# Optimization experiments

Hardware: AMD Instinct MI355X
Metric: run time of the kernel (lower is better)

The kernel has to match this reference:

```python
import jax, jax.numpy as jnp
import numpy as np

NUM_HEADS = 16

def setup_inputs() -> dict:
    key = jax.random.key(0)
    ks = jax.random.split(key, 5)
    b, n, d = 2, 2048, 1024
    s = 0.02
    return {
        "x": jax.random.normal(ks[0], (b, n, d), jnp.float32),
        "wq": jax.random.normal(ks[1], (d, d), jnp.float32) * s,
        "wk": jax.random.normal(ks[2], (d, d), jnp.float32) * s,
        "wv": jax.random.normal(ks[3], (d, d), jnp.float32) * s,
        "wo": jax.random.normal(ks[4], (d, d), jnp.float32) * s,
        "bo": jnp.zeros((d,), jnp.float32),
    }

def reference(x, wq, wk, wv, wo, bo):
    b, n, c = x.shape
    h = NUM_HEADS
    hd = c // h
    scale = hd ** -0.5
    # qkv projections (qkv_bias=False); torch Linear computes x @ W.T
    def split_heads(t):
        return t.reshape(b, n, h, hd).transpose(0, 2, 1, 3)  # b h n d
    q = split_heads(x @ wq.T)
    k = split_heads(x @ wk.T)
    v = split_heads(x @ wv.T)
    dots = jnp.einsum('bhid,bhjd->bhij', q, k) * scale
    attn = jax.nn.softmax(dots, axis=-1)  # attn_drop=0 -> identity
    out = jnp.einsum('bhij,bhjd->bhid', attn, v)
    out = out.transpose(0, 2, 1, 3).reshape(b, n, c)
    out = out @ wo.T + bo  # proj_drop=0 -> identity
    return out
```

## Files before the change

### kernel.cpp

```cpp
#include <hip/hip_runtime.h>
#include <hip/hip_bf16.h>

typedef float f32x4 __attribute__((ext_vector_type(4)));
typedef short short8 __attribute__((ext_vector_type(8)));
typedef short short4v __attribute__((ext_vector_type(4)));

#define MFMA(a, b, c) __builtin_amdgcn_mfma_f32_16x16x32_bf16((a), (b), (c), 0, 0, 0)

#if __has_builtin(__builtin_amdgcn_exp2f)
#define EXP2(x) __builtin_amdgcn_exp2f(x)
#else
#define EXP2(x) exp2f(x)
#endif

#define B_  2
#define N_  2048
#define C_  1024
#define H_  16
#define HD_ 64
#define M_  (B_ * N_)

#define QSCALE 0.18033688011112042f

typedef const __attribute__((address_space(1))) void* gp_t;
typedef __attribute__((address_space(3))) void* sp_t;
#define GLL16(g, s) __builtin_amdgcn_global_load_lds((gp_t)(const void*)(g), (sp_t)(void*)(s), 16, 0, 0)

__device__ __forceinline__ short f2bf(float f) {
    union { float fv; unsigned u; } v; v.fv = f;
    unsigned r = v.u + 0x7fffu + ((v.u >> 16) & 1u);
    return (short)(r >> 16);
}
__device__ __forceinline__ unsigned pack_rne(float a, float b) {
    return (unsigned)(unsigned short)f2bf(a) | ((unsigned)(unsigned short)f2bf(b) << 16);
}

__global__ __launch_bounds__(256) void convert_kernel(
    const float* __restrict__ x,  const float* __restrict__ wq,
    const float* __restrict__ wk, const float* __restrict__ wv,
    const float* __restrict__ wo, short* __restrict__ dst)
{
    size_t e = ((size_t)blockIdx.x * 256 + threadIdx.x) * 8;
    const float* src; size_t off;
    if (e < 4194304)      { src = x;  off = e; }
    else if (e < 5242880) { src = wq; off = e - 4194304; }
    else if (e < 6291456) { src = wk; off = e - 5242880; }
    else if (e < 7340032) { src = wv; off = e - 6291456; }
    else                  { src = wo; off = e - 7340032; }
    float4 a = *(const float4*)(src + off);
    float4 b = *(const float4*)(src + off + 4);
    short8 s;
    s[0] = f2bf(a.x); s[1] = f2bf(a.y); s[2] = f2bf(a.z); s[3] = f2bf(a.w);
    s[4] = f2bf(b.x); s[5] = f2bf(b.y); s[6] = f2bf(b.z); s[7] = f2bf(b.w);
    *(short8*)(dst + e) = s;
}

__global__ __launch_bounds__(256) void qkv_gemm(
    const short* __restrict__ xb, const short* __restrict__ Wb,
    short* __restrict__ Qb, short* __restrict__ Kb, short* __restrict__ Vt)
{
    const int m0 = blockIdx.x * 128;
    const int n0 = blockIdx.y * 128;
    __shared__ short As[128 * 32];
    __shared__ short Bs[128 * 32];
    const int tid  = threadIdx.x;
    const int wave = tid >> 6, lane = tid & 63;
    const int quad = lane >> 4, l16 = lane & 15;
    const int wr = (wave >> 1) * 64, wc = (wave & 1) * 64;

    f32x4 acc[4][4] = {};

    for (int kk = 0; kk < C_; kk += 32) {
        __syncthreads();
        #pragma unroll
        for (int it = 0; it < 2; ++it) {
            int f = (it * 256 + tid) * 8;
            int row = f >> 5, col = f & 31;
            GLL16(xb + (size_t)(m0 + row) * C_ + kk + col, &As[f]);
            GLL16(Wb + (size_t)(n0 + row) * C_ + kk + col, &Bs[f]);
        }
        __syncthreads();
        short8 af[4], bf[4];
        #pragma unroll
        for (int mi = 0; mi < 4; ++mi) af[mi] = *(const short8*)&As[(wr + mi * 16 + l16) * 32 + quad * 8];
        #pragma unroll
        for (int ni = 0; ni < 4; ++ni) bf[ni] = *(const short8*)&Bs[(wc + ni * 16 + l16) * 32 + quad * 8];
        #pragma unroll
        for (int mi = 0; mi < 4; ++mi)
        #pragma unroll
        for (int ni = 0; ni < 4; ++ni)
            acc[mi][ni] = MFMA(af[mi], bf[ni], acc[mi][ni]);
    }

    const int which = n0 >> 10;
    const int nb = n0 & 1023;
    #pragma unroll
    for (int mi = 0; mi < 4; ++mi)
    #pragma unroll
    for (int ni = 0; ni < 4; ++ni)
    #pragma unroll
    for (int r = 0; r < 4; ++r) {
        int m  = m0 + wr + mi * 16 + quad * 4 + r;
        int cc = nb + wc + ni * 16 + l16;
        float av = acc[mi][ni][r];
        if (which == 0) av *= QSCALE;
        short bv = f2bf(av);
        int bb = m >> 11, ns = m & (N_ - 1);
        int h = cc >> 6, d = cc & 63;
        size_t bh = (size_t)(bb * H_ + h);
        if (which == 0)      Qb[(bh * N_ + ns) * HD_ + d] = bv;
        else if (which == 1) Kb[(bh * N_ + ns) * HD_ + d] = bv;
        else                 Vt[(bh * HD_ + d) * N_ + ns] = bv;
    }
}

__global__ __launch_bounds__(256, 2) void attn_kernel(
    const short* __restrict__ Qb, const short* __restrict__ Kb,
    const short* __restrict__ Vt, short* __restrict__ Ob)
{
    const int bh = blockIdx.y;
    const int b = bh >> 4, h = bh & (H_ - 1);
    const int i0 = blockIdx.x * 128;
    __shared__ short Qs[128 * 64];
    __shared__ short Ks[2][64 * 64];
    __shared__ short Vs[2][64 * 64];
    const int tid  = threadIdx.x;
    const int wave = tid >> 6, lane = tid & 63;
    const int quad = lane >> 4, l16 = lane & 15;
    const int sw = l16 & 7;

    const short* Qg = Qb + ((size_t)bh * N_ + i0) * HD_;
    const short* Kg = Kb + (size_t)bh * N_ * HD_;
    const short* Vg = Vt + (size_t)bh * HD_ * N_;

    const int row0 = tid >> 3,  c0 = (tid & 7) ^ (row0 & 7);
    const int row1 = row0 + 32, c1 = (tid & 7) ^ (row1 & 7);
    const short* KgA0 = Kg + row0 * HD_ + c0 * 8;
    const short* KgA1 = Kg + row1 * HD_ + c1 * 8;
    const short* VgA0 = Vg + (size_t)row0 * N_ + c0 * 8;
    const short* VgA1 = Vg + (size_t)row1 * N_ + c1 * 8;

    #pragma unroll
    for (int it = 0; it < 4; ++it) {
        int s = it * 256 + tid;
        int row = s >> 3, c = (s & 7) ^ (row & 7);
        GLL16(Qg + row * HD_ + c * 8, &Qs[s * 8]);
    }
    GLL16(KgA0, &Ks[0][tid * 8]);
    GLL16(KgA1, &Ks[0][(tid + 256) * 8]);
    GLL16(VgA0, &Vs[0][tid * 8]);
    GLL16(VgA1, &Vs[0][(tid + 256) * 8]);
    __syncthreads();

    short8 qf[2][2];
    #pragma unroll
    for (int s = 0; s < 2; ++s) {
        int row = (wave * 32 + s * 16 + l16) * 64;
        qf[s][0] = *(const short8*)&Qs[row + ((quad ^ sw) * 8)];
        qf[s][1] = *(const short8*)&Qs[row + (((quad + 4) ^ sw) * 8)];
    }

    f32x4 o[2][4] = {};
    float lrow[2] = {0.f, 0.f};

    for (int jt = 0; jt < N_ / 64; ++jt) {
        const int cur = jt & 1;
        if (jt + 1 < N_ / 64) {
            int j1 = (jt + 1) * 64;
            GLL16(KgA0 + (size_t)j1 * HD_, &Ks[cur ^ 1][tid * 8]);
            GLL16(KgA1 + (size_t)j1 * HD_, &Ks[cur ^ 1][(tid + 256) * 8]);
            GLL16(VgA0 + j1, &Vs[cur ^ 1][tid * 8]);
            GLL16(VgA1 + j1, &Vs[cur ^ 1][(tid + 256) * 8]);
        }
        const short* Kc = Ks[cur];
        const short* Vc = Vs[cur];

        #pragma unroll
        for (int half = 0; half < 2; ++half) {
            unsigned pq[2][4];
            #pragma unroll
            for (int nio = 0; nio < 2; ++nio) {
                int ni = half * 2 + nio;
                int krow = (ni * 16 + l16) * 64;
                short8 kf0 = *(const short8*)&Kc[krow + ((quad ^ sw) * 8)];
                short8 kf1 = *(const short8*)&Kc[krow + (((quad + 4) ^ sw) * 8)];
                #pragma unroll
                for (int s = 0; s < 2; ++s) {
                    f32x4 st = {0.f, 0.f, 0.f, 0.f};
                    st = MFMA(kf0, qf[s][0], st);
                    st = MFMA(kf1, qf[s][1], st);
                    union { float f; unsigned u; } e0, e1, e2, e3;
                    e0.f = EXP2(st[0]); e1.f = EXP2(st[1]);
                    e2.f = EXP2(st[2]); e3.f = EXP2(st[3]);
                    lrow[s] += (e0.f + e1.f) + (e2.f + e3.f);
                    pq[s][nio * 2]     = (e0.u >> 16) | (e1.u & 0xffff0000u);
                    pq[s][nio * 2 + 1] = (e2.u >> 16) | (e3.u & 0xffff0000u);
                }
            }
            #pragma unroll
            for (int di = 0; di < 4; ++di) {
                int vrow = (di * 16 + l16) * 64;
                int ch1 = (half * 4 +     (quad >> 1)) ^ sw;
                int ch2 = (half * 4 + 2 + (quad >> 1)) ^ sw;
                union { struct { short4v lo, hi; } p; short8 v; } va;
                va.p.lo = *(const short4v*)&Vc[vrow + ch1 * 8 + (quad & 1) * 4];
                va.p.hi = *(const short4v*)&Vc[vrow + ch2 * 8 + (quad & 1) * 4];
                #pragma unroll
                for (int s = 0; s < 2; ++s) {
                    union { unsigned u[4]; short8 v; } pb;
                    pb.u[0] = pq[s][0]; pb.u[1] = pq[s][1];
                    pb.u[2] = pq[s][2]; pb.u[3] = pq[s][3];
                    o[s][di] = MFMA(va.v, pb.v, o[s][di]);
                }
            }
        }
        __syncthreads();
    }

    #pragma unroll
    for (int s = 0; s < 2; ++s) {
        float l = lrow[s];
        l += __shfl_xor(l, 16, 64);
        l += __shfl_xor(l, 32, 64);
        float inv = 1.f / l;
        int ig = i0 + wave * 32 + s * 16 + l16;
        size_t base = ((size_t)(b * N_ + ig)) * C_ + h * HD_;
        #pragma unroll
        for (int di = 0; di < 4; ++di) {
            unsigned p01 = pack_rne(o[s][di][0] * inv, o[s][di][1] * inv);
            unsigned p23 = pack_rne(o[s][di][2] * inv, o[s][di][3] * inv);
            *(unsigned*)&Ob[base + di * 16 + quad * 4]     = p01;
            *(unsigned*)&Ob[base + di * 16 + quad * 4 + 2] = p23;
        }
    }
}

__global__ __launch_bounds__(256) void proj_gemm(
    const short* __restrict__ Ob, const short* __restrict__ wob,
    const float* __restrict__ bo, float* __restrict__ out)
{
    const int m0 = blockIdx.x * 64;
    const int n0 = blockIdx.y * 128;
    __shared__ short As[64 * 32];
    __shared__ short Bs[128 * 32];
    const int tid  = threadIdx.x;
    const int wave = tid >> 6, lane = tid & 63;
    const int quad = lane >> 4, l16 = lane & 15;
    const int wr = (wave >> 1) * 32, wc = (wave & 1) * 64;

    f32x4 acc[2][4] = {};

    for (int kk = 0; kk < C_; kk += 32) {
        __syncthreads();
        {
            int f = tid * 8;
            int row = f >> 5, col = f & 31;
            GLL16(Ob + (size_t)(m0 + row) * C_ + kk + col, &As[f]);
        }
        #pragma unroll
        for (int it = 0; it < 2; ++it) {
            int f = (it * 256 + tid) * 8;
            int row = f >> 5, col = f & 31;
            GLL16(wob + (size_t)(n0 + row) * C_ + kk + col, &Bs[f]);
        }
        __syncthreads();
        short8 af[2], bf[4];
        #pragma unroll
        for (int mi = 0; mi < 2; ++mi) af[mi] = *(const short8*)&As[(wr + mi * 16 + l16) * 32 + quad * 8];
        #pragma unroll
        for (int ni = 0; ni < 4; ++ni) bf[ni] = *(const short8*)&Bs[(wc + ni * 16 + l16) * 32 + quad * 8];
        #pragma unroll
        for (int mi = 0; mi < 2; ++mi)
        #pragma unroll
        for (int ni = 0; ni < 4; ++ni)
            acc[mi][ni] = MFMA(af[mi], bf[ni], acc[mi][ni]);
    }

    #pragma unroll
    for (int mi = 0; mi < 2; ++mi)
    #pragma unroll
    for (int ni = 0; ni < 4; ++ni)
    #pragma unroll
    for (int r = 0; r < 4; ++r) {
        int m = m0 + wr + mi * 16 + quad * 4 + r;
        int c = n0 + wc + ni * 16 + l16;
        out[(size_t)m * C_ + c] = acc[mi][ni][r] + bo[c];
    }
}

extern "C" void kernel_launch(void* const* d_in, const int* in_sizes, int n_in,
                              void* d_out, int out_size, void* d_ws, size_t ws_size,
                              hipStream_t stream) {
    const float* x  = (const float*)d_in[0];
    const float* wq = (const float*)d_in[1];
    const float* wk = (const float*)d_in[2];
    const float* wv = (const float*)d_in[3];
    const float* wo = (const float*)d_in[4];
    const float* bo = (const float*)d_in[5];
    float* out = (float*)d_out;

    short* xb  = (short*)d_ws;
    short* Wb  = xb  + 4194304;
    short* wob = Wb  + 3145728;
    short* Qb  = wob + 1048576;
    short* Kb  = Qb  + 4194304;
    short* Vt  = Kb  + 4194304;
    short* Obuf= Vt  + 4194304;

    dim3 blk(256);
    convert_kernel<<<4096, blk, 0, stream>>>(x, wq, wk, wv, wo, xb);
    qkv_gemm<<<dim3(M_ / 128, 3072 / 128), blk, 0, stream>>>(xb, Wb, Qb, Kb, Vt);
    attn_kernel<<<dim3(N_ / 128, B_ * H_), blk, 0, stream>>>(Qb, Kb, Vt, Obuf);
    proj_gemm<<<dim3(M_ / 64, C_ / 128), blk, 0, stream>>>(Obuf, wob, bo, out);
}
```

Measured before the change: 190.9 us.

## Split attention over key halves and split-K the output projection

```diff
diff --git a/kernel.cpp b/kernel.cpp
--- a/kernel.cpp
+++ b/kernel.cpp
@@ -114,16 +114,19 @@
     }
 }
 
-__global__ __launch_bounds__(256, 2) void attn_kernel(
+__global__ __launch_bounds__(256, 4) void attn_kernel(
     const short* __restrict__ Qb, const short* __restrict__ Kb,
-    const short* __restrict__ Vt, short* __restrict__ Ob)
+    const short* __restrict__ Vt, short* __restrict__ op0,
+    short* __restrict__ op1, float* __restrict__ lb)
 {
     const int bh = blockIdx.y;
     const int b = bh >> 4, h = bh & (H_ - 1);
     const int i0 = blockIdx.x * 128;
-    __shared__ short Qs[128 * 64];
+    const int half = blockIdx.z;
+    const int jzb = half * (N_ / 2);
     __shared__ short Ks[2][64 * 64];
     __shared__ short Vs[2][64 * 64];
+    short* const Qs = &Ks[0][0];
     const int tid  = threadIdx.x;
     const int wave = tid >> 6, lane = tid & 63;
     const int quad = lane >> 4, l16 = lane & 15;
@@ -135,10 +138,10 @@
 
     const int row0 = tid >> 3,  c0 = (tid & 7) ^ (row0 & 7);
     const int row1 = row0 + 32, c1 = (tid & 7) ^ (row1 & 7);
-    const short* KgA0 = Kg + row0 * HD_ + c0 * 8;
-    const short* KgA1 = Kg + row1 * HD_ + c1 * 8;
-    const short* VgA0 = Vg + (size_t)row0 * N_ + c0 * 8;
-    const short* VgA1 = Vg + (size_t)row1 * N_ + c1 * 8;
+    const short* KgA0 = Kg + (size_t)(jzb + row0) * HD_ + c0 * 8;
+    const short* KgA1 = Kg + (size_t)(jzb + row1) * HD_ + c1 * 8;
+    const short* VgA0 = Vg + (size_t)row0 * N_ + jzb + c0 * 8;
+    const short* VgA1 = Vg + (size_t)row1 * N_ + jzb + c1 * 8;
 
     #pragma unroll
     for (int it = 0; it < 4; ++it) {
@@ -146,26 +149,29 @@
         int row = s >> 3, c = (s & 7) ^ (row & 7);
         GLL16(Qg + row * HD_ + c * 8, &Qs[s * 8]);
     }
+    __syncthreads();
+    short8 qf[2][2];
+    #pragma unroll
+    for (int s = 0; s < 2; ++s) {
+        int row = (wave * 32 + s * 16 + l16) * 64;
+        qf[s][0] = *(const short8*)&Qs[row + ((quad ^ sw) * 8)];
+        qf[s][1] = *(const short8*)&Qs[row + (((quad + 4) ^ sw) * 8)];
+    }
+    __syncthreads();
+
     GLL16(KgA0, &Ks[0][tid * 8]);
     GLL16(KgA1, &Ks[0][(tid + 256) * 8]);
     GLL16(VgA0, &Vs[0][tid * 8]);
     GLL16(VgA1, &Vs[0][(tid + 256) * 8]);
     __syncthreads();
 
-    short8 qf[2][2];
-    #pragma unroll
-    for (int s = 0; s < 2; ++s) {
-        int row = (wave * 32 + s * 16 + l16) * 64;
-        qf[s][0] = *(const short8*)&Qs[row + ((quad ^ sw) * 8)];
-        qf[s][1] = *(const short8*)&Qs[row + (((quad + 4) ^ sw) * 8)];
-    }
-
     f32x4 o[2][4] = {};
     float lrow[2] = {0.f, 0.f};
-
-    for (int jt = 0; jt < N_ / 64; ++jt) {
+    const int NT = (N_ / 2) / 64;
+
+    for (int jt = 0; jt < NT; ++jt) {
         const int cur = jt & 1;
-        if (jt + 1 < N_ / 64) {
+        if (jt + 1 < NT) {
             int j1 = (jt + 1) * 64;
             GLL16(KgA0 + (size_t)j1 * HD_, &Ks[cur ^ 1][tid * 8]);
             GLL16(KgA1 + (size_t)j1 * HD_, &Ks[cur ^ 1][(tid + 256) * 8]);
@@ -176,11 +182,11 @@
         const short* Vc = Vs[cur];
 
         #pragma unroll
-        for (int half = 0; half < 2; ++half) {
+        for (int hf = 0; hf < 2; ++hf) {
             unsigned pq[2][4];
             #pragma unroll
             for (int nio = 0; nio < 2; ++nio) {
-                int ni = half * 2 + nio;
+                int ni = hf * 2 + nio;
                 int krow = (ni * 16 + l16) * 64;
                 short8 kf0 = *(const short8*)&Kc[krow + ((quad ^ sw) * 8)];
                 short8 kf1 = *(const short8*)&Kc[krow + (((quad + 4) ^ sw) * 8)];
@@ -200,8 +206,8 @@
             #pragma unroll
             for (int di = 0; di < 4; ++di) {
                 int vrow = (di * 16 + l16) * 64;
-                int ch1 = (half * 4 +     (quad >> 1)) ^ sw;
-                int ch2 = (half * 4 + 2 + (quad >> 1)) ^ sw;
+                int ch1 = (hf * 4 +     (quad >> 1)) ^ sw;
+                int ch2 = (hf * 4 + 2 + (quad >> 1)) ^ sw;
                 union { struct { short4v lo, hi; } p; short8 v; } va;
                 va.p.lo = *(const short4v*)&Vc[vrow + ch1 * 8 + (quad & 1) * 4];
                 va.p.hi = *(const short4v*)&Vc[vrow + ch2 * 8 + (quad & 1) * 4];
@@ -217,22 +223,52 @@
         __syncthreads();
     }
 
+    short* __restrict__ oph = half ? op1 : op0;
+    float* __restrict__ lbh = lb + half * (B_ * H_ * N_);
     #pragma unroll
     for (int s = 0; s < 2; ++s) {
         float l = lrow[s];
         l += __shfl_xor(l, 16, 64);
         l += __shfl_xor(l, 32, 64);
-        float inv = 1.f / l;
         int ig = i0 + wave * 32 + s * 16 + l16;
+        if (quad == 0) lbh[bh * N_ + ig] = l;
         size_t base = ((size_t)(b * N_ + ig)) * C_ + h * HD_;
         #pragma unroll
         for (int di = 0; di < 4; ++di) {
-            unsigned p01 = pack_rne(o[s][di][0] * inv, o[s][di][1] * inv);
-            unsigned p23 = pack_rne(o[s][di][2] * inv, o[s][di][3] * inv);
-            *(unsigned*)&Ob[base + di * 16 + quad * 4]     = p01;
-            *(unsigned*)&Ob[base + di * 16 + quad * 4 + 2] = p23;
-        }
-    }
+            unsigned p01 = pack_rne(o[s][di][0], o[s][di][1]);
+            unsigned p23 = pack_rne(o[s][di][2], o[s][di][3]);
+            *(unsigned*)&oph[base + di * 16 + quad * 4]     = p01;
+            *(unsigned*)&oph[base + di * 16 + quad * 4 + 2] = p23;
+        }
+    }
+}
+
+__global__ __launch_bounds__(256) void combine_kernel(
+    const short* __restrict__ op0, const short* __restrict__ op1,
+    const float* __restrict__ lb, short* __restrict__ Ob)
+{
+    int e = blockIdx.x * 256 + threadIdx.x;
+    size_t base = (size_t)e * 8;
+    int iflat = (int)(base >> 10);
+    int col   = (int)(base & 1023);
+    int hh = col >> 6;
+    int bb = iflat >> 11, ii = iflat & (N_ - 1);
+    int lidx = (bb * H_ + hh) * N_ + ii;
+    float inv = 1.f / (lb[lidx] + lb[B_ * H_ * N_ + lidx]);
+
+    uint4 u0 = *(const uint4*)(op0 + base);
+    uint4 u1 = *(const uint4*)(op1 + base);
+    unsigned r[4];
+    const unsigned* a = (const unsigned*)&u0;
+    const unsigned* c = (const unsigned*)&u1;
+    #pragma unroll
+    for (int k = 0; k < 4; ++k) {
+        union { unsigned u; float f; } lo0, hi0, lo1, hi1;
+        lo0.u = a[k] << 16; hi0.u = a[k] & 0xffff0000u;
+        lo1.u = c[k] << 16; hi1.u = c[k] & 0xffff0000u;
+        r[k] = pack_rne((lo0.f + lo1.f) * inv, (hi0.f + hi1.f) * inv);
+    }
+    *(uint4*)(Ob + base) = *(uint4*)r;
 }
 
 __global__ __launch_bounds__(256) void proj_gemm(
@@ -241,6 +277,7 @@
 {
     const int m0 = blockIdx.x * 64;
     const int n0 = blockIdx.y * 128;
+    const int kz = blockIdx.z * (C_ / 2);
     __shared__ short As[64 * 32];
     __shared__ short Bs[128 * 32];
     const int tid  = threadIdx.x;
@@ -250,7 +287,8 @@
 
     f32x4 acc[2][4] = {};
 
-    for (int kk = 0; kk < C_; kk += 32) {
+    for (int kt = 0; kt < C_ / 64; ++kt) {
+        int kk = kz + kt * 32;
         __syncthreads();
         {
             int f = tid * 8;
@@ -284,7 +322,8 @@
     for (int r = 0; r < 4; ++r) {
         int m = m0 + wr + mi * 16 + quad * 4 + r;
         int c = n0 + wc + ni * 16 + l16;
-        out[(size_t)m * C_ + c] = acc[mi][ni][r] + bo[c];
+        float v = acc[mi][ni][r] + (blockIdx.z == 0 ? bo[c] : 0.f);
+        unsafeAtomicAdd(&out[(size_t)m * C_ + c], v);
     }
 }
 
@@ -306,10 +345,15 @@
     short* Kb  = Qb  + 4194304;
     short* Vt  = Kb  + 4194304;
     short* Obuf= Vt  + 4194304;
+    short* op0 = Obuf+ 4194304;
+    short* op1 = op0 + 4194304;
+    float* lbuf= (float*)(op1 + 4194304);
 
     dim3 blk(256);
     convert_kernel<<<4096, blk, 0, stream>>>(x, wq, wk, wv, wo, xb);
+    hipMemsetAsync(out, 0, (size_t)out_size * sizeof(float), stream);
     qkv_gemm<<<dim3(M_ / 128, 3072 / 128), blk, 0, stream>>>(xb, Wb, Qb, Kb, Vt);
-    attn_kernel<<<dim3(N_ / 128, B_ * H_), blk, 0, stream>>>(Qb, Kb, Vt, Obuf);
-    proj_gemm<<<dim3(M_ / 64, C_ / 128), blk, 0, stream>>>(Obuf, wob, bo, out);
-}
+    attn_kernel<<<dim3(N_ / 128, B_ * H_, 2), blk, 0, stream>>>(Qb, Kb, Vt, op0, op1, lbuf);
+    combine_kernel<<<2048, blk, 0, stream>>>(op0, op1, lbuf, Obuf);
+    proj_gemm<<<dim3(M_ / 64, C_ / 128, 2), blk, 0, stream>>>(Obuf, wob, bo, out);
+}
```

Result: slower. 214.4 us (+12.3%).
